# Performance work log

Hardware: AMD Instinct MI355X
Metric: run time of the kernel (lower is better)

The kernel has to match this reference:

```python
import jax, jax.numpy as jnp
import numpy as np

B, C, H, W = 16, 768, 32, 32
HEADS = 12
EPS = 1e-5


def _make_rel_index(h, w):
    coords = np.stack(np.meshgrid(np.arange(h), np.arange(w), indexing='ij'))  # [2,h,w]
    cf = coords.reshape(2, -1)                      # [2,N]
    rel = cf[:, :, None] - cf[:, None, :]           # [2,N,N]
    rel = rel.transpose(1, 2, 0).copy()             # [N,N,2]
    rel[:, :, 0] += h - 1
    rel[:, :, 1] += w - 1
    rel[:, :, 0] *= 2 * w - 1
    return jnp.asarray(rel.sum(-1), dtype=jnp.int32)  # [N,N]


def setup_inputs() -> dict:
    key = jax.random.key(0)
    ks = jax.random.split(key, 8)
    s = 0.02
    return {
        'x': jax.random.normal(ks[0], (B, C, H, W), jnp.float32),
        'rpb_table': jax.random.normal(ks[1], ((2 * H - 1) * (2 * W - 1), HEADS), jnp.float32) * s,
        'g1': jnp.ones((C,), jnp.float32),
        'b1': jnp.zeros((C,), jnp.float32),
        'q_w': jax.random.normal(ks[2], (C, C), jnp.float32) * s,
        'q_b': jnp.zeros((C,), jnp.float32),
        'kv_w': jax.random.normal(ks[3], (2 * C, C), jnp.float32) * s,
        'kv_b': jnp.zeros((2 * C,), jnp.float32),
        'proj_w': jax.random.normal(ks[4], (C, C), jnp.float32) * s,
        'proj_b': jnp.zeros((C,), jnp.float32),
        'g2': jnp.ones((C,), jnp.float32),
        'b2': jnp.zeros((C,), jnp.float32),
        'fc1_w': jax.random.normal(ks[5], (4 * C, C), jnp.float32) * s,
        'fc1_b': jnp.zeros((4 * C,), jnp.float32),
        'fc2_w': jax.random.normal(ks[6], (C, 4 * C), jnp.float32) * s,
        'fc2_b': jnp.zeros((C,), jnp.float32),
        'rel_index': _make_rel_index(H, W),
    }


def _ln(t, g, b):
    m = t.mean(-1, keepdims=True)
    v = ((t - m) ** 2).mean(-1, keepdims=True)
    return (t - m) * jax.lax.rsqrt(v + EPS) * g + b


def reference(x, rpb_table, g1, b1, q_w, q_b, kv_w, kv_b, proj_w, proj_b,
              g2, b2, fc1_w, fc1_b, fc2_w, fc2_b, rel_index):
    b, c, h, w = x.shape
    n = h * w
    heads = rpb_table.shape[1]
    hd = c // heads
    scale = hd ** -0.5

    xt = x.reshape(b, c, n).transpose(0, 2, 1)  # [B,N,C]

    # --- attention branch ---
    xn = _ln(xt, g1, b1)
    q = (xn @ q_w.T + q_b).reshape(b, n, heads, hd).transpose(0, 2, 1, 3)  # [B,h,N,d]
    kv = (xn @ kv_w.T + kv_b).reshape(b, n, 2, heads, hd)
    k = kv[:, :, 0].transpose(0, 2, 1, 3)  # [B,h,N,d]
    v = kv[:, :, 1].transpose(0, 2, 1, 3)  # [B,h,N,d]
    attn = jnp.einsum('bhnd,bhmd->bhnm', q, k) * scale  # [B,h,N,N]
    bias = rpb_table[rel_index].transpose(2, 0, 1)      # [h,N,N]
    attn = jax.nn.softmax(attn + bias[None], axis=-1)
    o = jnp.einsum('bhnm,bhmd->bhnd', attn, v).transpose(0, 2, 1, 3).reshape(b, n, c)
    o = o @ proj_w.T + proj_b
    xt = xt + o

    # --- mlp branch ---
    xn = _ln(xt, g2, b2)
    h1 = jax.nn.gelu(xn @ fc1_w.T + fc1_b, approximate=False)
    xt = xt + (h1 @ fc2_w.T + fc2_b)

    return xt.transpose(0, 2, 1).reshape(b, c, h, w)
```

## Files before the change

kernel.cpp:

```cpp
#include <hip/hip_runtime.h>
#include <hip/hip_bf16.h>
#include <math.h>

typedef unsigned short u16;
typedef unsigned int u32;
typedef float f32x4 __attribute__((ext_vector_type(4)));
typedef short bf16x8 __attribute__((ext_vector_type(8)));
typedef unsigned short us4 __attribute__((ext_vector_type(4)));

struct alignas(16) F4 { float v[4]; };
template <int N> struct Tag { static constexpr int v = N; };

static constexpr int Bb = 16;
static constexpr int Cc = 768;
static constexpr int Nn = 1024;
static constexpr int NH = 12;
static constexpr int HD = 64;
static constexpr float LOG2E = 1.4426950408889634f;

static __device__ __forceinline__ u16 f2bf(float f) {
  union { float f; unsigned u; } v; v.f = f;
  unsigned u = v.u;
  u += 0x7fffu + ((u >> 16) & 1u);
  return (u16)(u >> 16);
}
static __device__ __forceinline__ float bf2f(u16 x) {
  union { unsigned u; float f; } v; v.u = ((unsigned)x) << 16; return v.f;
}
static __device__ __forceinline__ void gload16(const u16* g, u16* l) {
  __builtin_amdgcn_global_load_lds((const __attribute__((address_space(1))) u32*)g,
                                   (__attribute__((address_space(3))) u32*)l, 16, 0, 0);
}

__global__ __launch_bounds__(256) void k_prep(const float* __restrict__ q_w,
    const float* __restrict__ kv_w, const float* __restrict__ proj_w,
    const float* __restrict__ fc1_w, const float* __restrict__ fc2_w,
    const float* __restrict__ q_b, const float* __restrict__ kv_b,
    u16* __restrict__ wqkv, u16* __restrict__ wproj, u16* __restrict__ wfc1,
    u16* __restrict__ wfc2, float* __restrict__ bqkv) {
  int i = blockIdx.x * 256 + threadIdx.x;
  if (i < 589824)            wqkv[i] = f2bf(q_w[i]);
  else if (i < 1769472)      wqkv[i] = f2bf(kv_w[i - 589824]);
  else if (i < 2359296)      wproj[i - 1769472] = f2bf(proj_w[i - 1769472]);
  else if (i < 4718592)      wfc1[i - 2359296] = f2bf(fc1_w[i - 2359296]);
  else if (i < 7077888)      wfc2[i - 4718592] = f2bf(fc2_w[i - 4718592]);
  else if (i < 7078656)      bqkv[i - 7077888] = q_b[i - 7077888];
  else                       bqkv[i - 7077888] = kv_b[i - 7078656];
}

__global__ void k_transpose(const float* __restrict__ x, float* __restrict__ xt) {
  __shared__ float tile[32][33];
  int b = blockIdx.z, c0 = blockIdx.y * 32, n0 = blockIdx.x * 32;
  int tx = threadIdx.x, ty = threadIdx.y;
  const float* xp = x + (size_t)b * Cc * Nn;
  #pragma unroll
  for (int i = 0; i < 32; i += 8)
    tile[ty + i][tx] = xp[(size_t)(c0 + ty + i) * Nn + n0 + tx];
  __syncthreads();
  float* xtp = xt + (size_t)b * Nn * Cc;
  #pragma unroll
  for (int i = 0; i < 32; i += 8)
    xtp[(size_t)(n0 + ty + i) * Cc + c0 + tx] = tile[tx][ty + i];
}

__global__ __launch_bounds__(256) void k_layernorm(const float* __restrict__ in,
    const float* __restrict__ gam, const float* __restrict__ bet,
    u16* __restrict__ out) {
  int wave = threadIdx.x >> 6, lane = threadIdx.x & 63;
  int row = blockIdx.x * 4 + wave;
  const float* p = in + (size_t)row * Cc;
  float v[12]; float s = 0.f;
  #pragma unroll
  for (int i = 0; i < 12; i++) { v[i] = p[lane + i * 64]; s += v[i]; }
  #pragma unroll
  for (int m = 32; m >= 1; m >>= 1) s += __shfl_xor(s, m);
  float mean = s * (1.f / 768.f);
  float q = 0.f;
  #pragma unroll
  for (int i = 0; i < 12; i++) { float d = v[i] - mean; q += d * d; }
  #pragma unroll
  for (int m = 32; m >= 1; m >>= 1) q += __shfl_xor(q, m);
  float rstd = rsqrtf(q * (1.f / 768.f) + 1e-5f);
  u16* o = out + (size_t)row * Cc;
  #pragma unroll
  for (int i = 0; i < 12; i++) {
    int j = lane + i * 64;
    o[j] = f2bf((v[i] - mean) * rstd * gam[j] + bet[j]);
  }
}

__global__ void k_bias_pre(const float* __restrict__ rpb, const int* __restrict__ rel,
                           u16* __restrict__ out) {
  int idx = blockIdx.x * 256 + threadIdx.x;
  int k = idx & 1023, q = (idx >> 10) & 1023, h = idx >> 20;
  float v = rpb[rel[(size_t)q * Nn + k] * NH + h];
  out[((size_t)h * Nn + q) * Nn + k] = f2bf(v * LOG2E);
}

struct GemmArgs {
  const u16* A; const u16* W; const float* bias;
  int M, N, K;
  const float* resIn;
  float* outF;
  u16* outBf;
  u16 *q, *k, *v;
};

template <int EPI>
__global__ __launch_bounds__(512, 2) void k_gemm(GemmArgs p) {
  extern __shared__ f32x4 smv[];
  u16* lA = (u16*)smv;
  u16* lB = (u16*)smv + 2 * 256 * 64;
  const int tid = threadIdx.x;
  const int wave = tid >> 6, lane = tid & 63;
  const int l15 = lane & 15, g = lane >> 4, h7 = l15 & 7;
  const int wr = wave >> 2, wc = wave & 3;
  const int rl = tid >> 3, cc8 = tid & 7;
  const int nwg = gridDim.x * gridDim.y;
  const int wg = blockIdx.y * gridDim.x + blockIdx.x;
  const int swz = (wg & 7) * (nwg >> 3) + (wg >> 3);
  const int bn = (swz % gridDim.x) * 256, bm = (swz / gridDim.x) * 256;
  const int K = p.K;

  f32x4 acc[8][4];
  #pragma unroll
  for (int i = 0; i < 8; i++)
    #pragma unroll
    for (int j = 0; j < 4; j++) acc[i][j] = (f32x4){0.f, 0.f, 0.f, 0.f};

  const u16* Ab = p.A + (size_t)bm * K;
  const u16* Wb = p.W + (size_t)bn * K;
  const int csw = (cc8 ^ (rl & 7)) * 8;

  auto stageA = [&](int buf, int k0, int half) {
    int r0 = half * 64 + rl, r1 = r0 + 128;
    gload16(Ab + (size_t)r0 * K + k0 + csw, &lA[buf * 16384 + r0 * 64 + cc8 * 8]);
    gload16(Ab + (size_t)r1 * K + k0 + csw, &lA[buf * 16384 + r1 * 64 + cc8 * 8]);
  };
  auto stageB = [&](int buf, int k0, int half) {
    int r0 = ((rl >> 5) << 6) + half * 32 + (rl & 31), r1 = r0 + 128;
    gload16(Wb + (size_t)r0 * K + k0 + csw, &lB[buf * 16384 + r0 * 64 + cc8 * 8]);
    gload16(Wb + (size_t)r1 * K + k0 + csw, &lB[buf * 16384 + r1 * 64 + cc8 * 8]);
  };

  bf16x8 a[4][2], bq[4][2];
  auto rdA = [&](int buf, int mt, int kk) {
    int row = wr * 128 + mt * 16 + l15;
    return *(const bf16x8*)&lA[buf * 16384 + row * 64 + (((kk << 2) + g) ^ h7) * 8];
  };
  auto rdB = [&](int buf, int nt, int kk) {
    int row = wc * 64 + nt * 16 + l15;
    return *(const bf16x8*)&lB[buf * 16384 + row * 64 + (((kk << 2) + g) ^ h7) * 8];
  };
  auto MF = [&](auto MBt, auto NBt) {
    constexpr int MB = decltype(MBt)::v, NB = decltype(NBt)::v;
    __builtin_amdgcn_s_setprio(1);
    #pragma unroll
    for (int kk = 0; kk < 2; kk++)
      #pragma unroll
      for (int mi = 0; mi < 4; mi++)
        #pragma unroll
        for (int ni = 0; ni < 2; ni++)
          acc[MB + mi][NB + ni] = __builtin_amdgcn_mfma_f32_16x16x32_bf16(
              a[mi][kk], bq[NB + ni][kk], acc[MB + mi][NB + ni], 0, 0, 0);
    __builtin_amdgcn_s_setprio(0);
  };

  stageA(0, 0, 0); stageB(0, 0, 0); stageB(0, 0, 1); stageA(0, 0, 1);
  stageA(1, 64, 0);
  asm volatile("s_waitcnt vmcnt(6)" ::: "memory");
  __builtin_amdgcn_s_barrier();

  auto TILE = [&](int t, auto tag) {
    constexpr int TAIL = decltype(tag)::v;
    const int buf = t & 1, nb = buf ^ 1;
    const int k1 = (t + 1) * 64;
    #pragma unroll
    for (int mi = 0; mi < 4; mi++) { a[mi][0] = rdA(buf, mi, 0); a[mi][1] = rdA(buf, mi, 1); }
    #pragma unroll
    for (int ni = 0; ni < 2; ni++) { bq[ni][0] = rdB(buf, ni, 0); bq[ni][1] = rdB(buf, ni, 1); }
    if constexpr (TAIL < 2) {
      stageB(nb, k1, 0);
      asm volatile("s_waitcnt vmcnt(6)" ::: "memory");
    } else {
      asm volatile("s_waitcnt vmcnt(2)" ::: "memory");
    }
    __builtin_amdgcn_s_barrier();
    __builtin_amdgcn_sched_barrier(0);
    MF(Tag<0>{}, Tag<0>{});
    #pragma unroll
    for (int ni = 0; ni < 2; ni++) { bq[2 + ni][0] = rdB(buf, 2 + ni, 0); bq[2 + ni][1] = rdB(buf, 2 + ni, 1); }
    if constexpr (TAIL < 2) {
      stageB(nb, k1, 1);
      asm volatile("s_waitcnt vmcnt(6)" ::: "memory");
    } else {
      asm volatile("s_waitcnt vmcnt(0)" ::: "memory");
    }
    __builtin_amdgcn_s_barrier();
    __builtin_amdgcn_sched_barrier(0);
    MF(Tag<0>{}, Tag<2>{});
    #pragma unroll
    for (int mi = 0; mi < 4; mi++) { a[mi][0] = rdA(buf, 4 + mi, 0); a[mi][1] = rdA(buf, 4 + mi, 1); }
    if constexpr (TAIL < 2) stageA(nb, k1, 1);
    __builtin_amdgcn_s_barrier();
    __builtin_amdgcn_sched_barrier(0);
    MF(Tag<4>{}, Tag<2>{});
    if constexpr (TAIL == 0) {
      stageA(buf, k1 + 64, 0);
      asm volatile("s_waitcnt vmcnt(6)" ::: "memory");
    } else if constexpr (TAIL == 1) {
      asm volatile("s_waitcnt vmcnt(4)" ::: "memory");
    }
    __builtin_amdgcn_s_barrier();
    __builtin_amdgcn_sched_barrier(0);
    MF(Tag<4>{}, Tag<0>{});
  };

  const int NT = K >> 6;
  for (int t = 0; t < NT - 2; ++t) TILE(t, Tag<0>{});
  TILE(NT - 2, Tag<1>{});
  TILE(NT - 1, Tag<2>{});

  #pragma unroll
  for (int mt = 0; mt < 8; mt++) {
    int rowb = bm + wr * 128 + mt * 16 + g * 4;
    #pragma unroll
    for (int nt = 0; nt < 4; nt++) {
      int col = bn + wc * 64 + nt * 16 + l15;
      float bias = p.bias[col];
      if constexpr (EPI == 0) {
        #pragma unroll
        for (int r = 0; r < 4; r++) {
          int grow = rowb + r;
          int bb = grow >> 10, nnq = grow & 1023;
          float val = acc[mt][nt][r] + bias;
          if (col < 768) {
            int head = col >> 6, d = col & 63;
            p.q[(((size_t)bb * NH + head) * Nn + nnq) * HD + d] = f2bf(val * (0.125f * LOG2E));
          } else {
            int j2 = col - 768;
            if (j2 < 768) {
              int head = j2 >> 6, d = j2 & 63;
              p.k[(((size_t)bb * NH + head) * Nn + nnq) * HD + d] = f2bf(val);
            } else {
              int j3 = j2 - 768;
              int head = j3 >> 6, d = j3 & 63;
              p.v[(((size_t)bb * NH + head) * HD + d) * Nn + nnq] = f2bf(val);
            }
          }
        }
      } else if constexpr (EPI == 1) {
        #pragma unroll
        for (int r = 0; r < 4; r++) {
          size_t idx = (size_t)(rowb + r) * p.N + col;
          p.outF[idx] = acc[mt][nt][r] + bias + p.resIn[idx];
        }
      } else if constexpr (EPI == 2) {
        #pragma unroll
        for (int r = 0; r < 4; r++) {
          float val = acc[mt][nt][r] + bias;
          val = 0.5f * val * (1.f + erff(val * 0.70710678118654752f));
          p.outBf[(size_t)(rowb + r) * p.N + col] = f2bf(val);
        }
      } else {
        int bb = rowb >> 10, n0 = rowb & 1023;
        F4 ov;
        #pragma unroll
        for (int r = 0; r < 4; r++)
          ov.v[r] = acc[mt][nt][r] + bias + p.resIn[(size_t)(rowb + r) * Cc + col];
        *(F4*)&p.outF[((size_t)bb * Cc + col) * Nn + n0] = ov;
      }
    }
  }
}

__global__ __launch_bounds__(512, 6) void k_attn(const u16* __restrict__ qt,
    const u16* __restrict__ kt_, const u16* __restrict__ vtt,
    const u16* __restrict__ bias2, u16* __restrict__ o) {
  __shared__ __align__(16) u16 lK[2][64 * 64];
  __shared__ __align__(16) u16 lV[2][64 * 64];
  __shared__ __align__(16) u16 lP[8][16 * 64];
  const int tid = threadIdx.x, wave = tid >> 6, lane = tid & 63;
  const int l15 = lane & 15, g = lane >> 4;
  const int b = blockIdx.z, h = blockIdx.y;
  const int q0 = blockIdx.x * 128 + wave * 16;
  const size_t bh  = ((size_t)b * NH + h) * Nn * HD;
  const size_t bhT = ((size_t)b * NH + h) * HD * Nn;
  const u16* biasH = bias2 + (size_t)h * Nn * Nn;
  u16* myP = &lP[wave][0];
  const float THR = 8.f * LOG2E;
  const int sRow = tid >> 3, sCol = tid & 7;
  const int h7 = l15 & 7;

  bf16x8 qa0, qa1;
  {
    const u16* qp = qt + bh + (size_t)(q0 + l15) * HD + g * 8;
    qa0 = *(const bf16x8*)qp;
    qa1 = *(const bf16x8*)(qp + 32);
  }
  f32x4 ao[4];
  float mr = -1e30f, lr = 0.f;
  #pragma unroll
  for (int d = 0; d < 4; d++) ao[d] = (f32x4){0.f, 0.f, 0.f, 0.f};

  auto issueKV = [&](int kt0, int buf) {
    int cs = (sCol ^ (sRow & 7)) << 3;
    gload16(kt_ + bh + (size_t)(kt0 + sRow) * HD + cs, &lK[buf][sRow * 64 + sCol * 8]);
    gload16(vtt + bhT + (size_t)sRow * Nn + kt0 + cs, &lV[buf][sRow * 64 + sCol * 8]);
  };

  issueKV(0, 0);
  for (int t = 0; t < 16; ++t) {
    const int kt0 = t * 64, buf = t & 1;
    asm volatile("s_waitcnt vmcnt(0) lgkmcnt(0)" ::: "memory");
    __builtin_amdgcn_s_barrier();
    __builtin_amdgcn_sched_barrier(0);
    if (t < 15) issueKV(kt0 + 64, buf ^ 1);

    us4 bvv[4];
    #pragma unroll
    for (int nt = 0; nt < 4; nt++)
      bvv[nt] = *(const us4*)(biasH + (size_t)(q0 + l15) * Nn + kt0 + nt * 16 + g * 4);

    f32x4 s[4];
    __builtin_amdgcn_s_setprio(1);
    #pragma unroll
    for (int nt = 0; nt < 4; nt++) {
      const int row = nt * 16 + l15;
      bf16x8 kb0 = *(const bf16x8*)&lK[buf][row * 64 + ((g ^ h7) << 3)];
      bf16x8 kb1 = *(const bf16x8*)&lK[buf][row * 64 + (((g + 4) ^ h7) << 3)];
      s[nt] = __builtin_amdgcn_mfma_f32_16x16x32_bf16(kb0, qa0,
                (f32x4){0.f, 0.f, 0.f, 0.f}, 0, 0, 0);
      s[nt] = __builtin_amdgcn_mfma_f32_16x16x32_bf16(kb1, qa1, s[nt], 0, 0, 0);
    }
    __builtin_amdgcn_s_setprio(0);

    #pragma unroll
    for (int nt = 0; nt < 4; nt++) {
      #pragma unroll
      for (int r = 0; r < 4; r++) s[nt][r] += bf2f(bvv[nt][r]);
    }
    float pm = fmaxf(fmaxf(s[0][0], s[0][1]), fmaxf(s[0][2], s[0][3]));
    #pragma unroll
    for (int nt = 1; nt < 4; nt++)
      pm = fmaxf(pm, fmaxf(fmaxf(s[nt][0], s[nt][1]), fmaxf(s[nt][2], s[nt][3])));
    pm = fmaxf(pm, __shfl_xor(pm, 16));
    pm = fmaxf(pm, __shfl_xor(pm, 32));
    if (__any(pm > mr + THR)) {
      float mnew = fmaxf(mr, pm);
      float fac = __builtin_amdgcn_exp2f(mr - mnew);
      lr *= fac;
      mr = mnew;
      f32x4 facO;
      #pragma unroll
      for (int r = 0; r < 4; r++) facO[r] = __shfl(fac, g * 4 + r);
      #pragma unroll
      for (int d = 0; d < 4; d++) ao[d] *= facO;
    }
    float ps = 0.f;
    #pragma unroll
    for (int nt = 0; nt < 4; nt++) {
      #pragma unroll
      for (int r = 0; r < 4; r++) {
        float pv = __builtin_amdgcn_exp2f(s[nt][r] - mr);
        s[nt][r] = pv;
        ps += pv;
      }
    }
    ps += __shfl_xor(ps, 16);
    ps += __shfl_xor(ps, 32);
    lr += ps;
    #pragma unroll
    for (int nt = 0; nt < 4; nt++) {
      u32 w0 = (u32)f2bf(s[nt][0]) | ((u32)f2bf(s[nt][1]) << 16);
      u32 w1 = (u32)f2bf(s[nt][2]) | ((u32)f2bf(s[nt][3]) << 16);
      int cbase = (((2 * nt + (g >> 1)) ^ h7) << 3) + (g & 1) * 4;
      *(u32*)&myP[l15 * 64 + cbase]     = w0;
      *(u32*)&myP[l15 * 64 + cbase + 2] = w1;
    }
    __builtin_amdgcn_s_setprio(1);
    #pragma unroll
    for (int kc = 0; kc < 2; kc++) {
      bf16x8 pa = *(const bf16x8*)&myP[l15 * 64 + (((4 * kc + g) ^ h7) << 3)];
      #pragma unroll
      for (int d = 0; d < 4; d++) {
        const int rv = d * 16 + l15;
        bf16x8 vb = *(const bf16x8*)&lV[buf][rv * 64 + (((kc * 4 + g) ^ h7) << 3)];
        ao[d] = __builtin_amdgcn_mfma_f32_16x16x32_bf16(pa, vb, ao[d], 0, 0, 0);
      }
    }
    __builtin_amdgcn_s_setprio(0);
  }
  f32x4 linv;
  #pragma unroll
  for (int r = 0; r < 4; r++) linv[r] = 1.f / __shfl(lr, g * 4 + r);
  #pragma unroll
  for (int r = 0; r < 4; r++) {
    int qg = q0 + g * 4 + r;
    u16* op = o + ((size_t)b * Nn + qg) * Cc + h * HD;
    #pragma unroll
    for (int d = 0; d < 4; d++)
      op[d * 16 + l15] = f2bf(ao[d][r] * linv[r]);
  }
}

extern "C" void kernel_launch(void* const* d_in, const int* in_sizes, int n_in,
                              void* d_out, int out_size, void* d_ws, size_t ws_size,
                              hipStream_t stream) {
  const float* x      = (const float*)d_in[0];
  const float* rpb    = (const float*)d_in[1];
  const float* g1     = (const float*)d_in[2];
  const float* b1v    = (const float*)d_in[3];
  const float* q_w    = (const float*)d_in[4];
  const float* q_b    = (const float*)d_in[5];
  const float* kv_w   = (const float*)d_in[6];
  const float* kv_b   = (const float*)d_in[7];
  const float* proj_w = (const float*)d_in[8];
  const float* proj_b = (const float*)d_in[9];
  const float* g2     = (const float*)d_in[10];
  const float* b2v    = (const float*)d_in[11];
  const float* fc1_w  = (const float*)d_in[12];
  const float* fc1_b  = (const float*)d_in[13];
  const float* fc2_w  = (const float*)d_in[14];
  const float* fc2_b  = (const float*)d_in[15];
  const int*   rel    = (const int*)d_in[16];
  float* out = (float*)d_out;

  char* ws = (char*)d_ws;
  size_t off = 0;
  auto alloc = [&](size_t bytes) -> void* {
    void* p = ws + off;
    off += (bytes + 255) & ~(size_t)255;
    return p;
  };
  u16*   wqkv  = (u16*)alloc((size_t)2304 * 768 * 2);
  u16*   wproj = (u16*)alloc((size_t)768 * 768 * 2);
  u16*   wfc1  = (u16*)alloc((size_t)3072 * 768 * 2);
  u16*   wfc2  = (u16*)alloc((size_t)768 * 3072 * 2);
  float* bqkv  = (float*)alloc((size_t)2304 * 4);
  float* xt    = (float*)alloc((size_t)16384 * 768 * 4);
  float* xt2   = (float*)alloc((size_t)16384 * 768 * 4);
  u16*   xn    = (u16*)alloc((size_t)16384 * 768 * 2);
  u16*   qb_   = (u16*)alloc((size_t)Bb * NH * Nn * HD * 2);
  u16*   kb_   = (u16*)alloc((size_t)Bb * NH * Nn * HD * 2);
  u16*   vb_   = (u16*)alloc((size_t)Bb * NH * Nn * HD * 2);
  u16*   ob_   = (u16*)alloc((size_t)16384 * 768 * 2);
  u16*   h1    = qb_;
  u16*   bias2 = (u16*)xt2;

  hipFuncSetAttribute((const void*)k_gemm<0>, hipFuncAttributeMaxDynamicSharedMemorySize, 131072);
  hipFuncSetAttribute((const void*)k_gemm<1>, hipFuncAttributeMaxDynamicSharedMemorySize, 131072);
  hipFuncSetAttribute((const void*)k_gemm<2>, hipFuncAttributeMaxDynamicSharedMemorySize, 131072);
  hipFuncSetAttribute((const void*)k_gemm<3>, hipFuncAttributeMaxDynamicSharedMemorySize, 131072);

  k_prep<<<27657, 256, 0, stream>>>(q_w, kv_w, proj_w, fc1_w, fc2_w, q_b, kv_b,
                                    wqkv, wproj, wfc1, wfc2, bqkv);

  k_transpose<<<dim3(32, 24, 16), dim3(32, 8), 0, stream>>>(x, xt);
  k_layernorm<<<4096, 256, 0, stream>>>(xt, g1, b1v, xn);
  k_bias_pre<<<49152, 256, 0, stream>>>(rpb, rel, bias2);

  GemmArgs ga = {};
  ga.A = xn; ga.W = wqkv; ga.bias = bqkv; ga.M = 16384; ga.N = 2304; ga.K = 768;
  ga.q = qb_; ga.k = kb_; ga.v = vb_;
  k_gemm<0><<<dim3(9, 64), 512, 131072, stream>>>(ga);

  k_attn<<<dim3(8, NH, Bb), 512, 0, stream>>>(qb_, kb_, vb_, bias2, ob_);

  GemmArgs gp = {};
  gp.A = ob_; gp.W = wproj; gp.bias = proj_b; gp.M = 16384; gp.N = 768; gp.K = 768;
  gp.resIn = xt; gp.outF = xt2;
  k_gemm<1><<<dim3(3, 64), 512, 131072, stream>>>(gp);

  k_layernorm<<<4096, 256, 0, stream>>>(xt2, g2, b2v, xn);

  GemmArgs gf1 = {};
  gf1.A = xn; gf1.W = wfc1; gf1.bias = fc1_b; gf1.M = 16384; gf1.N = 3072; gf1.K = 768;
  gf1.outBf = h1;
  k_gemm<2><<<dim3(12, 64), 512, 131072, stream>>>(gf1);

  GemmArgs gf2 = {};
  gf2.A = h1; gf2.W = wfc2; gf2.bias = fc2_b; gf2.M = 16384; gf2.N = 768; gf2.K = 3072;
  gf2.resIn = xt2; gf2.outF = out;
  k_gemm<3><<<dim3(3, 64), 512, 131072, stream>>>(gf2);
}
```

Baseline: 574.2 us.

## Prefetch attention bias a tile ahead and split K/V load waits

The relative-position bias loads move out of the critical path. They are now issued one key tile ahead into double-buffered registers, and the loop is unrolled by two so the buffers alternate. The single full vmcnt(0) wait becomes a partial wait for K before QK^T and a second wait plus barrier for V before the PV MFMAs, so V loads can overlap the softmax. The probability packing also switches to the hardware v_cvt_pk_bf16_f32 instruction. In exchange there is one extra barrier per tile and more register pressure, and correctness depends on hand-counted vmcnt values.

```diff
diff --git a/kernel.cpp b/kernel.cpp
--- a/kernel.cpp
+++ b/kernel.cpp
@@ -308,19 +308,28 @@
     gload16(kt_ + bh + (size_t)(kt0 + sRow) * HD + cs, &lK[buf][sRow * 64 + sCol * 8]);
     gload16(vtt + bhT + (size_t)sRow * Nn + kt0 + cs, &lV[buf][sRow * 64 + sCol * 8]);
   };
-
+  auto issueBias = [&](int kt0, us4* bv) {
+    #pragma unroll
+    for (int nt = 0; nt < 4; nt++)
+      bv[nt] = *(const us4*)(biasH + (size_t)(q0 + l15) * Nn + kt0 + nt * 16 + g * 4);
+  };
+
+  us4 bvA[4], bvB[4];
+  issueBias(0, bvA);
+  __builtin_amdgcn_sched_barrier(0);
   issueKV(0, 0);
-  for (int t = 0; t < 16; ++t) {
+
+  auto tile = [&](int t, us4* bvC, us4* bvN) {
     const int kt0 = t * 64, buf = t & 1;
-    asm volatile("s_waitcnt vmcnt(0) lgkmcnt(0)" ::: "memory");
+    asm volatile("s_waitcnt vmcnt(1)" ::: "memory");
     __builtin_amdgcn_s_barrier();
     __builtin_amdgcn_sched_barrier(0);
-    if (t < 15) issueKV(kt0 + 64, buf ^ 1);
-
-    us4 bvv[4];
-    #pragma unroll
-    for (int nt = 0; nt < 4; nt++)
-      bvv[nt] = *(const us4*)(biasH + (size_t)(q0 + l15) * Nn + kt0 + nt * 16 + g * 4);
+    if (t < 15) {
+      issueBias(kt0 + 64, bvN);
+      __builtin_amdgcn_sched_barrier(0);
+      issueKV(kt0 + 64, buf ^ 1);
+    }
+    __builtin_amdgcn_sched_barrier(0);
 
     f32x4 s[4];
     __builtin_amdgcn_s_setprio(1);
@@ -338,7 +347,7 @@
     #pragma unroll
     for (int nt = 0; nt < 4; nt++) {
       #pragma unroll
-      for (int r = 0; r < 4; r++) s[nt][r] += bf2f(bvv[nt][r]);
+      for (int r = 0; r < 4; r++) s[nt][r] += bf2f(bvC[nt][r]);
     }
     float pm = fmaxf(fmaxf(s[0][0], s[0][1]), fmaxf(s[0][2], s[0][3]));
     #pragma unroll
@@ -372,12 +381,17 @@
     lr += ps;
     #pragma unroll
     for (int nt = 0; nt < 4; nt++) {
-      u32 w0 = (u32)f2bf(s[nt][0]) | ((u32)f2bf(s[nt][1]) << 16);
-      u32 w1 = (u32)f2bf(s[nt][2]) | ((u32)f2bf(s[nt][3]) << 16);
+      u32 w0, w1;
+      asm("v_cvt_pk_bf16_f32 %0, %1, %2" : "=v"(w0) : "v"(s[nt][0]), "v"(s[nt][1]));
+      asm("v_cvt_pk_bf16_f32 %0, %1, %2" : "=v"(w1) : "v"(s[nt][2]), "v"(s[nt][3]));
       int cbase = (((2 * nt + (g >> 1)) ^ h7) << 3) + (g & 1) * 4;
       *(u32*)&myP[l15 * 64 + cbase]     = w0;
       *(u32*)&myP[l15 * 64 + cbase + 2] = w1;
     }
+    if (t < 15) asm volatile("s_waitcnt vmcnt(6)" ::: "memory");
+    else        asm volatile("s_waitcnt vmcnt(0)" ::: "memory");
+    __builtin_amdgcn_s_barrier();
+    __builtin_amdgcn_sched_barrier(0);
     __builtin_amdgcn_s_setprio(1);
     #pragma unroll
     for (int kc = 0; kc < 2; kc++) {
@@ -390,7 +404,14 @@
       }
     }
     __builtin_amdgcn_s_setprio(0);
+  };
+
+  #pragma unroll 1
+  for (int t = 0; t < 16; t += 2) {
+    tile(t, bvA, bvB);
+    tile(t + 1, bvB, bvA);
   }
+
   f32x4 linv;
   #pragma unroll
   for (int r = 0; r < 4; r++) linv[r] = 1.f / __shfl(lr, g * 4 + r);
```

Result: slower. 694.5 us (+21.0%).

## Prefetch bias one tile ahead and split K/V waits in attention loop

Applied to the files above, without the earlier changes.

Restructures the flash-attention main loop so the relative-position bias for the next tile is loaded into registers one iteration early (ping-pong bvA/bvB), and the K and V async LDS loads get separate partial vmcnt waits. The QK^T stage now only waits for K, and V is waited on just before the PV MFMAs, with a second barrier. The bf16 packing also uses the hardware v_cvt_pk_bf16_f32 instruction instead of software rounding. This aims to hide global bias and V load latency behind compute, at the cost of an extra barrier per tile and fragile hand-counted vmcnt values.

```diff
diff --git a/kernel.cpp b/kernel.cpp
--- a/kernel.cpp
+++ b/kernel.cpp
@@ -274,6 +274,102 @@
   }
 }
 
+#define ATTN_ISSUE_KV(kt0_, buf_)                                                 \
+  { gload16(kt_ + bh + (size_t)((kt0_) + sRow) * HD + csKV,                       \
+            &lK[buf_][sRow * 64 + sCol * 8]);                                     \
+    gload16(vtt + bhT + (size_t)sRow * Nn + (kt0_) + csKV,                        \
+            &lV[buf_][sRow * 64 + sCol * 8]); }
+
+#define ATTN_ISSUE_BIAS(kt0_, BV)                                                 \
+  { const u16* bp_ = biasH + (size_t)(q0 + l15) * Nn + (kt0_) + g * 4;            \
+    BV[0] = *(const us4*)bp_;        BV[1] = *(const us4*)(bp_ + 16);             \
+    BV[2] = *(const us4*)(bp_ + 32); BV[3] = *(const us4*)(bp_ + 48); }
+
+#define ATTN_TILE(t_, BVC, BVN)                                                   \
+  { const int kt0 = (t_) * 64, buf = (t_) & 1;                                    \
+    asm volatile("s_waitcnt vmcnt(1)" ::: "memory");                              \
+    __builtin_amdgcn_s_barrier();                                                 \
+    __builtin_amdgcn_sched_barrier(0);                                            \
+    if ((t_) < 15) {                                                              \
+      ATTN_ISSUE_BIAS(kt0 + 64, BVN);                                             \
+      __builtin_amdgcn_sched_barrier(0);                                          \
+      ATTN_ISSUE_KV(kt0 + 64, buf ^ 1);                                           \
+    }                                                                             \
+    __builtin_amdgcn_sched_barrier(0);                                            \
+    f32x4 s[4];                                                                   \
+    __builtin_amdgcn_s_setprio(1);                                                \
+    _Pragma("unroll")                                                             \
+    for (int nt = 0; nt < 4; nt++) {                                              \
+      const int row = nt * 16 + l15;                                              \
+      bf16x8 kb0 = *(const bf16x8*)&lK[buf][row * 64 + ((g ^ h7) << 3)];          \
+      bf16x8 kb1 = *(const bf16x8*)&lK[buf][row * 64 + (((g + 4) ^ h7) << 3)];    \
+      s[nt] = __builtin_amdgcn_mfma_f32_16x16x32_bf16(kb0, qa0,                   \
+                (f32x4){0.f, 0.f, 0.f, 0.f}, 0, 0, 0);                            \
+      s[nt] = __builtin_amdgcn_mfma_f32_16x16x32_bf16(kb1, qa1, s[nt], 0, 0, 0);  \
+    }                                                                             \
+    __builtin_amdgcn_s_setprio(0);                                                \
+    _Pragma("unroll")                                                             \
+    for (int nt = 0; nt < 4; nt++) {                                              \
+      _Pragma("unroll")                                                           \
+      for (int r = 0; r < 4; r++) s[nt][r] += bf2f(BVC[nt][r]);                   \
+    }                                                                             \
+    float pm = fmaxf(fmaxf(s[0][0], s[0][1]), fmaxf(s[0][2], s[0][3]));           \
+    _Pragma("unroll")                                                             \
+    for (int nt = 1; nt < 4; nt++)                                                \
+      pm = fmaxf(pm, fmaxf(fmaxf(s[nt][0], s[nt][1]), fmaxf(s[nt][2], s[nt][3])));\
+    pm = fmaxf(pm, __shfl_xor(pm, 16));                                           \
+    pm = fmaxf(pm, __shfl_xor(pm, 32));                                           \
+    if (__any(pm > mr + THR)) {                                                   \
+      float mnew = fmaxf(mr, pm);                                                 \
+      float fac = __builtin_amdgcn_exp2f(mr - mnew);                              \
+      lr *= fac;                                                                  \
+      mr = mnew;                                                                  \
+      f32x4 facO;                                                                 \
+      _Pragma("unroll")                                                           \
+      for (int r = 0; r < 4; r++) facO[r] = __shfl(fac, g * 4 + r);               \
+      _Pragma("unroll")                                                           \
+      for (int d = 0; d < 4; d++) ao[d] *= facO;                                  \
+    }                                                                             \
+    float ps = 0.f;                                                               \
+    _Pragma("unroll")                                                             \
+    for (int nt = 0; nt < 4; nt++) {                                              \
+      _Pragma("unroll")                                                           \
+      for (int r = 0; r < 4; r++) {                                               \
+        float pv = __builtin_amdgcn_exp2f(s[nt][r] - mr);                         \
+        s[nt][r] = pv;                                                            \
+        ps += pv;                                                                 \
+      }                                                                           \
+    }                                                                             \
+    ps += __shfl_xor(ps, 16);                                                     \
+    ps += __shfl_xor(ps, 32);                                                     \
+    lr += ps;                                                                     \
+    _Pragma("unroll")                                                             \
+    for (int nt = 0; nt < 4; nt++) {                                              \
+      u32 w0, w1;                                                                 \
+      asm("v_cvt_pk_bf16_f32 %0, %1, %2" : "=v"(w0) : "v"(s[nt][0]), "v"(s[nt][1]));\
+      asm("v_cvt_pk_bf16_f32 %0, %1, %2" : "=v"(w1) : "v"(s[nt][2]), "v"(s[nt][3]));\
+      int cbase = (((2 * nt + (g >> 1)) ^ h7) << 3) + (g & 1) * 4;                \
+      *(u32*)&myP[l15 * 64 + cbase]     = w0;                                     \
+      *(u32*)&myP[l15 * 64 + cbase + 2] = w1;                                     \
+    }                                                                             \
+    if ((t_) < 15) asm volatile("s_waitcnt vmcnt(6)" ::: "memory");               \
+    else           asm volatile("s_waitcnt vmcnt(0)" ::: "memory");               \
+    __builtin_amdgcn_s_barrier();                                                 \
+    __builtin_amdgcn_sched_barrier(0);                                            \
+    __builtin_amdgcn_s_setprio(1);                                                \
+    _Pragma("unroll")                                                             \
+    for (int kc = 0; kc < 2; kc++) {                                              \
+      bf16x8 pa = *(const bf16x8*)&myP[l15 * 64 + (((4 * kc + g) ^ h7) << 3)];    \
+      _Pragma("unroll")                                                           \
+      for (int d = 0; d < 4; d++) {                                               \
+        const int rv = d * 16 + l15;                                              \
+        bf16x8 vb = *(const bf16x8*)&lV[buf][rv * 64 + (((kc * 4 + g) ^ h7) << 3)];\
+        ao[d] = __builtin_amdgcn_mfma_f32_16x16x32_bf16(pa, vb, ao[d], 0, 0, 0);  \
+      }                                                                           \
+    }                                                                             \
+    __builtin_amdgcn_s_setprio(0);                                                \
+  }
+
 __global__ __launch_bounds__(512, 6) void k_attn(const u16* __restrict__ qt,
     const u16* __restrict__ kt_, const u16* __restrict__ vtt,
     const u16* __restrict__ bias2, u16* __restrict__ o) {
@@ -291,6 +387,7 @@
   const float THR = 8.f * LOG2E;
   const int sRow = tid >> 3, sCol = tid & 7;
   const int h7 = l15 & 7;
+  const int csKV = (sCol ^ (sRow & 7)) << 3;
 
   bf16x8 qa0, qa1;
   {
@@ -303,94 +400,17 @@
   #pragma unroll
   for (int d = 0; d < 4; d++) ao[d] = (f32x4){0.f, 0.f, 0.f, 0.f};
 
-  auto issueKV = [&](int kt0, int buf) {
-    int cs = (sCol ^ (sRow & 7)) << 3;
-    gload16(kt_ + bh + (size_t)(kt0 + sRow) * HD + cs, &lK[buf][sRow * 64 + sCol * 8]);
-    gload16(vtt + bhT + (size_t)sRow * Nn + kt0 + cs, &lV[buf][sRow * 64 + sCol * 8]);
-  };
-
-  issueKV(0, 0);
-  for (int t = 0; t < 16; ++t) {
-    const int kt0 = t * 64, buf = t & 1;
-    asm volatile("s_waitcnt vmcnt(0) lgkmcnt(0)" ::: "memory");
-    __builtin_amdgcn_s_barrier();
-    __builtin_amdgcn_sched_barrier(0);
-    if (t < 15) issueKV(kt0 + 64, buf ^ 1);
-
-    us4 bvv[4];
-    #pragma unroll
-    for (int nt = 0; nt < 4; nt++)
-      bvv[nt] = *(const us4*)(biasH + (size_t)(q0 + l15) * Nn + kt0 + nt * 16 + g * 4);
-
-    f32x4 s[4];
-    __builtin_amdgcn_s_setprio(1);
-    #pragma unroll
-    for (int nt = 0; nt < 4; nt++) {
-      const int row = nt * 16 + l15;
-      bf16x8 kb0 = *(const bf16x8*)&lK[buf][row * 64 + ((g ^ h7) << 3)];
-      bf16x8 kb1 = *(const bf16x8*)&lK[buf][row * 64 + (((g + 4) ^ h7) << 3)];
-      s[nt] = __builtin_amdgcn_mfma_f32_16x16x32_bf16(kb0, qa0,
-                (f32x4){0.f, 0.f, 0.f, 0.f}, 0, 0, 0);
-      s[nt] = __builtin_amdgcn_mfma_f32_16x16x32_bf16(kb1, qa1, s[nt], 0, 0, 0);
-    }
-    __builtin_amdgcn_s_setprio(0);
-
-    #pragma unroll
-    for (int nt = 0; nt < 4; nt++) {
-      #pragma unroll
-      for (int r = 0; r < 4; r++) s[nt][r] += bf2f(bvv[nt][r]);
-    }
-    float pm = fmaxf(fmaxf(s[0][0], s[0][1]), fmaxf(s[0][2], s[0][3]));
-    #pragma unroll
-    for (int nt = 1; nt < 4; nt++)
-      pm = fmaxf(pm, fmaxf(fmaxf(s[nt][0], s[nt][1]), fmaxf(s[nt][2], s[nt][3])));
-    pm = fmaxf(pm, __shfl_xor(pm, 16));
-    pm = fmaxf(pm, __shfl_xor(pm, 32));
-    if (__any(pm > mr + THR)) {
-      float mnew = fmaxf(mr, pm);
-      float fac = __builtin_amdgcn_exp2f(mr - mnew);
-      lr *= fac;
-      mr = mnew;
-      f32x4 facO;
-      #pragma unroll
-      for (int r = 0; r < 4; r++) facO[r] = __shfl(fac, g * 4 + r);
-      #pragma unroll
-      for (int d = 0; d < 4; d++) ao[d] *= facO;
-    }
-    float ps = 0.f;
-    #pragma unroll
-    for (int nt = 0; nt < 4; nt++) {
-      #pragma unroll
-      for (int r = 0; r < 4; r++) {
-        float pv = __builtin_amdgcn_exp2f(s[nt][r] - mr);
-        s[nt][r] = pv;
-        ps += pv;
-      }
-    }
-    ps += __shfl_xor(ps, 16);
-    ps += __shfl_xor(ps, 32);
-    lr += ps;
-    #pragma unroll
-    for (int nt = 0; nt < 4; nt++) {
-      u32 w0 = (u32)f2bf(s[nt][0]) | ((u32)f2bf(s[nt][1]) << 16);
-      u32 w1 = (u32)f2bf(s[nt][2]) | ((u32)f2bf(s[nt][3]) << 16);
-      int cbase = (((2 * nt + (g >> 1)) ^ h7) << 3) + (g & 1) * 4;
-      *(u32*)&myP[l15 * 64 + cbase]     = w0;
-      *(u32*)&myP[l15 * 64 + cbase + 2] = w1;
-    }
-    __builtin_amdgcn_s_setprio(1);
-    #pragma unroll
-    for (int kc = 0; kc < 2; kc++) {
-      bf16x8 pa = *(const bf16x8*)&myP[l15 * 64 + (((4 * kc + g) ^ h7) << 3)];
-      #pragma unroll
-      for (int d = 0; d < 4; d++) {
-        const int rv = d * 16 + l15;
-        bf16x8 vb = *(const bf16x8*)&lV[buf][rv * 64 + (((kc * 4 + g) ^ h7) << 3)];
-        ao[d] = __builtin_amdgcn_mfma_f32_16x16x32_bf16(pa, vb, ao[d], 0, 0, 0);
-      }
-    }
-    __builtin_amdgcn_s_setprio(0);
+  us4 bvA[4], bvB[4];
+  ATTN_ISSUE_BIAS(0, bvA);
+  __builtin_amdgcn_sched_barrier(0);
+  ATTN_ISSUE_KV(0, 0);
+
+  #pragma unroll 1
+  for (int t = 0; t < 16; t += 2) {
+    ATTN_TILE(t, bvA, bvB);
+    ATTN_TILE(t + 1, bvB, bvA);
   }
+
   f32x4 linv;
   #pragma unroll
   for (int r = 0; r < 4; r++) linv[r] = 1.f / __shfl(lr, g * 4 + r);
```

After: 643.8 us. 12.1% more time.
